# Kernel optimization log

Measured on AMD Instinct MI355X. Metric: run time of the kernel, lower is better.

The kernel has to match this reference:

```python
import jax, jax.numpy as jnp
import numpy as np

DIM = 256
NUM_HEADS = 8
WINDOW = 8


def setup_inputs() -> dict:
    key = jax.random.key(0)
    k1, k2, k3 = jax.random.split(key, 3)
    x = jax.random.normal(k1, (4, DIM, 256, 256), dtype=jnp.float32)
    w_qkv = jax.random.normal(k2, (3 * DIM, DIM), dtype=jnp.float32) * 0.02
    w_proj = jax.random.normal(k3, (DIM, DIM), dtype=jnp.float32) * 0.02
    return {"x": x, "w_qkv": w_qkv, "w_proj": w_proj}


def reference(x, w_qkv, w_proj):
    B, C, H, W = x.shape
    ws = WINDOW
    nh = NUM_HEADS
    hd = C // nh
    scale = float(hd) ** -0.5

    pad_h = (ws - H % ws) % ws
    pad_w = (ws - W % ws) % ws
    if pad_h or pad_w:
        x = jnp.pad(x, ((0, 0), (0, 0), (0, pad_h), (0, pad_w)))
    Hp, Wp = H + pad_h, W + pad_w
    nHw, nWw = Hp // ws, Wp // ws
    N = ws * ws

    # 1x1 conv QKV projection (no bias): [3C,C] x [B,C,Hp,Wp]
    qkv = jnp.einsum('oc,bchw->bohw', w_qkv, x)
    q, k, v = jnp.split(qkv, 3, axis=1)

    def partition(t):
        # [B,C,Hp,Wp] -> [B*nHw*nWw, nh, N, hd]
        t = t.reshape(B, nh, hd, nHw, ws, nWw, ws)
        t = t.transpose(0, 3, 5, 1, 4, 6, 2)  # B,nHw,nWw,nh,ws,ws,hd
        return t.reshape(B * nHw * nWw, nh, N, hd)

    qw = partition(q)
    kw = partition(k)
    vw = partition(v)

    attn = jnp.einsum('whnd,whmd->whnm', qw, kw) * scale
    attn = jax.nn.softmax(attn, axis=-1)
    out = jnp.einsum('whnm,whmd->whnd', attn, vw)  # [Bn, nh, N, hd]

    # unpartition: [Bn,nh,N,hd] -> [B,C,Hp,Wp]
    out = out.reshape(B, nHw, nWw, nh, ws, ws, hd)
    out = out.transpose(0, 3, 6, 1, 4, 2, 5)  # B,nh,hd,nHw,ws,nWw,ws
    out = out.reshape(B, C, Hp, Wp)

    out = jnp.einsum('oc,bchw->bohw', w_proj, out)
    if pad_h:
        out = out[:, :, :H, :]
    if pad_w:
        out = out[:, :, :, :W]
    return out
```

## Files before the change

kernel.cpp:

```cpp
#include <hip/hip_runtime.h>


#define DIMC 256
#define NH   8
#define HD   32
#define WS   8
#define NTOK 64
#define HRES 256
#define IMG  (HRES * HRES)

#define XPITCH 272

typedef _Float16 f16x8 __attribute__((ext_vector_type(8)));
typedef _Float16 f16x4 __attribute__((ext_vector_type(4)));
typedef float    f32x4 __attribute__((ext_vector_type(4)));

#define MFMA(a, b, c) __builtin_amdgcn_mfma_f32_16x16x32_f16((a), (b), (c), 0, 0, 0)

__global__ __launch_bounds__(256) void cvt_weights(const float* __restrict__ wqkv,
                                                   const float* __restrict__ wproj,
                                                   _Float16* __restrict__ wq,
                                                   _Float16* __restrict__ wp)
{
    int i = blockIdx.x * 256 + threadIdx.x;
    const int NQ = 768 * 256;
    const int NT = NQ + 256 * 256;
    if (i < NQ)      wq[i] = (_Float16)wqkv[i];
    else if (i < NT) wp[i - NQ] = (_Float16)wproj[i - NQ];
}

template <int PRE>
__device__ __forceinline__ f16x8 ldw(const void* w, int idx)
{
    if constexpr (PRE) {
        return *(const f16x8*)((const _Float16*)w + idx);
    } else {
        const float* p = (const float*)w + idx;
        f16x8 r;
        #pragma unroll
        for (int j = 0; j < 8; ++j) r[j] = (_Float16)p[j];
        return r;
    }
}

__device__ __forceinline__ int2 shfl2(int2 v, int s)
{
    v.x = __shfl(v.x, s);
    v.y = __shfl(v.y, s);
    return v;
}

__device__ __forceinline__ int2 pack4(f32x4 a)
{
    f16x4 h;
    h[0] = (_Float16)a[0]; h[1] = (_Float16)a[1];
    h[2] = (_Float16)a[2]; h[3] = (_Float16)a[3];
    return __builtin_bit_cast(int2, h);
}

__device__ __forceinline__ f16x8 cat8(int2 lo, int2 hi)
{
    int4 w = {lo.x, lo.y, hi.x, hi.y};
    return __builtin_bit_cast(f16x8, w);
}

__device__ __forceinline__ f16x8 bfrag(int2 pu0, int2 pu1, int ln, int lq)
{
    const int slo = ln + 32 * (lq & 1);
    int2 l0 = shfl2(pu0, slo), h0 = shfl2(pu0, slo + 16);
    int2 l1 = shfl2(pu1, slo), h1 = shfl2(pu1, slo + 16);
    int2 lo = (lq & 2) ? l1 : l0;
    int2 hi = (lq & 2) ? h1 : h0;
    return cat8(lo, hi);
}

template <int PRE>
__global__ __launch_bounds__(512, 4)
void win_attn_mfma(const float* __restrict__ x,
                   const void* __restrict__ wqkv,
                   const void* __restrict__ wproj,
                   float* __restrict__ out)
{
    __shared__ _Float16 x_t[NTOK][XPITCH];
    __shared__ _Float16 ao_t[NTOK][XPITCH];

    const int t  = threadIdx.x;
    const int ln = t & 15;
    const int lq = (t & 63) >> 4;
    const int gu = __builtin_amdgcn_readfirstlane(t >> 6);

    const int lin = blockIdx.x + (blockIdx.y << 5) + (blockIdx.z << 10);
    const int w   = ((lin & 7) << 9) | (lin >> 3);
    const int b   = w >> 10;
    const int y0  = ((w >> 5) & 31) * WS;
    const int x0  = (w & 31) * WS;

    const f32x4 zero = {0.f, 0.f, 0.f, 0.f};
    const float scale = 0.17677669529663687f;

    {
        const int py = t & 7;
        const int cg = (t & 63) >> 3;
        const float* xb = x + (long)b * DIMC * IMG + (long)(y0 + py) * HRES + x0;
        #pragma unroll
        for (int i = 0; i < 4; ++i) {
            const int cbase = i * 64 + gu * 8;
            const float* src = xb + (long)(cbase + cg) * IMG;
            float4 f0 = *(const float4*)src;
            float4 f1 = *(const float4*)(src + 4);
            float v[8] = {f0.x, f0.y, f0.z, f0.w, f1.x, f1.y, f1.z, f1.w};
            #pragma unroll
            for (int s = 1; s < 8; s <<= 1) {
                float nv[8];
                #pragma unroll
                for (int j = 0; j < 8; ++j) {
                    float ex = __shfl_xor(v[j ^ s], 8 * s);
                    nv[j] = ((j ^ cg) & s) ? ex : v[j];
                }
                #pragma unroll
                for (int j = 0; j < 8; ++j) v[j] = nv[j];
            }
            f16x8 hv;
            #pragma unroll
            for (int j = 0; j < 8; ++j) hv[j] = (_Float16)v[j];
            *(f16x8*)&x_t[8 * py + cg][cbase] = hv;
        }
    }
    __syncthreads();

    int2 Qp[2][4], Kp[2][4], Vp[4][2];
    #pragma unroll
    for (int mt = 0; mt < 2; ++mt) {
        f32x4 aq[4], ak[4], av[4];
        #pragma unroll
        for (int nt = 0; nt < 4; ++nt) { aq[nt] = zero; ak[nt] = zero; av[nt] = zero; }
        const int rq = (          gu * HD + 16 * mt + ln) * DIMC;
        const int rk = (DIMC    + gu * HD + 16 * mt + ln) * DIMC;
        const int rv = (2 * DIMC + gu * HD + 16 * mt + ln) * DIMC;
        #pragma unroll
        for (int ks = 0; ks < 8; ++ks) {
            const int co = 32 * ks + 8 * lq;
            f16x8 wqf = ldw<PRE>(wqkv, rq + co);
            f16x8 wkf = ldw<PRE>(wqkv, rk + co);
            f16x8 wvf = ldw<PRE>(wqkv, rv + co);
            #pragma unroll
            for (int nt = 0; nt < 4; ++nt) {
                f16x8 xf = *(const f16x8*)&x_t[16 * nt + ln][co];
                aq[nt] = MFMA(wqf, xf, aq[nt]);
                ak[nt] = MFMA(wkf, xf, ak[nt]);
                av[nt] = MFMA(xf, wvf, av[nt]);
            }
        }
        #pragma unroll
        for (int nt = 0; nt < 4; ++nt) {
            Qp[mt][nt] = pack4(aq[nt] * scale);
            Kp[mt][nt] = pack4(ak[nt]);
            Vp[nt][mt] = pack4(av[nt]);
        }
    }

    {
        f16x8 kf[4], qf[4];
        #pragma unroll
        for (int kt = 0; kt < 4; ++kt) kf[kt] = bfrag(Kp[0][kt], Kp[1][kt], ln, lq);
        #pragma unroll
        for (int qt = 0; qt < 4; ++qt) qf[qt] = bfrag(Qp[0][qt], Qp[1][qt], ln, lq);

        f32x4 s[4][4];
        #pragma unroll
        for (int kt = 0; kt < 4; ++kt)
            #pragma unroll
            for (int qt = 0; qt < 4; ++qt)
                s[kt][qt] = MFMA(kf[kt], qf[qt], zero);

        float inv[4];
        #pragma unroll
        for (int qt = 0; qt < 4; ++qt) {
            float m = -1e30f;
            #pragma unroll
            for (int kt = 0; kt < 4; ++kt)
                #pragma unroll
                for (int r = 0; r < 4; ++r) m = fmaxf(m, s[kt][qt][r]);
            m = fmaxf(m, __shfl_xor(m, 16));
            m = fmaxf(m, __shfl_xor(m, 32));
            float sum = 0.f;
            #pragma unroll
            for (int kt = 0; kt < 4; ++kt)
                #pragma unroll
                for (int r = 0; r < 4; ++r) {
                    float e = __expf(s[kt][qt][r] - m);
                    s[kt][qt][r] = e;
                    sum += e;
                }
            sum += __shfl_xor(sum, 16);
            sum += __shfl_xor(sum, 32);
            inv[qt] = 1.f / sum;
        }

        int2 Pp[4][4];
        #pragma unroll
        for (int kt = 0; kt < 4; ++kt)
            #pragma unroll
            for (int qt = 0; qt < 4; ++qt)
                Pp[kt][qt] = pack4(s[kt][qt] * inv[qt]);

        f32x4 pv[2][4];
        #pragma unroll
        for (int dt = 0; dt < 2; ++dt)
            #pragma unroll
            for (int qt = 0; qt < 4; ++qt) pv[dt][qt] = zero;
        #pragma unroll
        for (int ks = 0; ks < 2; ++ks) {
            f16x8 vf[2], pf[4];
            #pragma unroll
            for (int dt = 0; dt < 2; ++dt)
                vf[dt] = bfrag(Vp[2 * ks][dt], Vp[2 * ks + 1][dt], ln, lq);
            #pragma unroll
            for (int qt = 0; qt < 4; ++qt)
                pf[qt] = bfrag(Pp[2 * ks][qt], Pp[2 * ks + 1][qt], ln, lq);
            #pragma unroll
            for (int dt = 0; dt < 2; ++dt)
                #pragma unroll
                for (int qt = 0; qt < 4; ++qt)
                    pv[dt][qt] = MFMA(vf[dt], pf[qt], pv[dt][qt]);
        }

        #pragma unroll
        for (int dt = 0; dt < 2; ++dt)
            #pragma unroll
            for (int qt = 0; qt < 4; ++qt) {
                f16x4 hv;
                #pragma unroll
                for (int r = 0; r < 4; ++r) hv[r] = (_Float16)pv[dt][qt][r];
                *(f16x4*)&ao_t[16 * qt + ln][gu * HD + 16 * dt + 4 * lq] = hv;
            }
    }
    __syncthreads();

    f32x4 fa[2][4];
    #pragma unroll
    for (int o = 0; o < 2; ++o)
        #pragma unroll
        for (int nt = 0; nt < 4; ++nt) fa[o][nt] = zero;
    {
        const int r0 = (16 * (2 * gu + 0) + ln) * DIMC;
        const int r1 = (16 * (2 * gu + 1) + ln) * DIMC;
        #pragma unroll
        for (int ks = 0; ks < 8; ++ks) {
            const int co = 32 * ks + 8 * lq;
            f16x8 w0 = ldw<PRE>(wproj, r0 + co);
            f16x8 w1 = ldw<PRE>(wproj, r1 + co);
            #pragma unroll
            for (int nt = 0; nt < 4; ++nt) {
                f16x8 af = *(const f16x8*)&ao_t[16 * nt + ln][co];
                fa[0][nt] = MFMA(w0, af, fa[0][nt]);
                fa[1][nt] = MFMA(w1, af, fa[1][nt]);
            }
        }
    }

    {
        float* ob = out + (long)b * DIMC * IMG + (long)y0 * HRES + x0;
        #pragma unroll
        for (int o = 0; o < 2; ++o)
            #pragma unroll
            for (int nt = 0; nt < 4; ++nt) {
                const int och = 16 * (2 * gu + o) + 4 * lq;
                const int tok = 16 * nt + ln;
                float* op = ob + (long)och * IMG + (tok >> 3) * HRES + (tok & 7);
                #pragma unroll
                for (int r = 0; r < 4; ++r) op[(long)r * IMG] = fa[o][nt][r];
            }
    }
}

extern "C" void kernel_launch(void* const* d_in, const int* in_sizes, int n_in,
                              void* d_out, int out_size, void* d_ws, size_t ws_size,
                              hipStream_t stream)
{
    const float* x      = (const float*)d_in[0];
    const float* w_qkv  = (const float*)d_in[1];
    const float* w_proj = (const float*)d_in[2];
    float* out          = (float*)d_out;

    dim3 grid(HRES / WS, HRES / WS, 4);
    dim3 block(512);

    const size_t need = (size_t)(768 * 256 + 256 * 256) * sizeof(_Float16);
    if (d_ws && ws_size >= need) {
        _Float16* wq = (_Float16*)d_ws;
        _Float16* wp = wq + 768 * 256;
        hipLaunchKernelGGL(cvt_weights, dim3(1024), dim3(256), 0, stream,
                           w_qkv, w_proj, wq, wp);
        hipLaunchKernelGGL((win_attn_mfma<1>), grid, block, 0, stream,
                           x, (const void*)wq, (const void*)wp, out);
    } else {
        hipLaunchKernelGGL((win_attn_mfma<0>), grid, block, 0, stream,
                           x, (const void*)w_qkv, (const void*)w_proj, out);
    }
}
```

Before: 1.013 ms.

## Process two adjacent windows per block with shared swizzled LDS buffer

Each block now handles two horizontally adjacent 8x8 windows, which halves the grid. The QKV weight fragments are reloaded per window, but the output-projection weights are loaded once and applied to 128 tokens. The separate x and attention-output LDS arrays are merged into one XOR-swizzled buffer that the attention output overwrites in place, and the global x loads and output stores now span 16 contiguous floats per row. In exchange, more register pressure from the doubled projection accumulators and extra barriers between the per-window phases may reduce overlap.

```diff
diff --git a/kernel.cpp b/kernel.cpp
--- a/kernel.cpp
+++ b/kernel.cpp
@@ -4,12 +4,10 @@
 #define DIMC 256
 #define NH   8
 #define HD   32
-#define WS   8
-#define NTOK 64
+#define NTOK2 128
 #define HRES 256
 #define IMG  (HRES * HRES)
-
-#define XPITCH 272
+#define XP   264
 
 typedef _Float16 f16x8 __attribute__((ext_vector_type(8)));
 typedef _Float16 f16x4 __attribute__((ext_vector_type(4)));
@@ -74,6 +72,11 @@
     return cat8(lo, hi);
 }
 
+__device__ __forceinline__ int swz(int row, int col)
+{
+    return row * XP + (col ^ (((row >> 3) & 7) << 3));
+}
+
 template <int PRE>
 __global__ __launch_bounds__(512, 4)
 void win_attn_mfma(const float* __restrict__ x,
@@ -81,31 +84,31 @@
                    const void* __restrict__ wproj,
                    float* __restrict__ out)
 {
-    __shared__ _Float16 x_t[NTOK][XPITCH];
-    __shared__ _Float16 ao_t[NTOK][XPITCH];
+    __shared__ _Float16 xa[NTOK2 * XP];
 
     const int t  = threadIdx.x;
     const int ln = t & 15;
     const int lq = (t & 63) >> 4;
     const int gu = __builtin_amdgcn_readfirstlane(t >> 6);
 
-    const int lin = blockIdx.x + (blockIdx.y << 5) + (blockIdx.z << 10);
-    const int w   = ((lin & 7) << 9) | (lin >> 3);
-    const int b   = w >> 10;
-    const int y0  = ((w >> 5) & 31) * WS;
-    const int x0  = (w & 31) * WS;
+    const int lin = blockIdx.x + (blockIdx.y << 4) + (blockIdx.z << 9);
+    const int w   = ((lin & 7) << 8) | (lin >> 3);
+    const int b   = w >> 9;
+    const int y0  = ((w >> 4) & 31) * 8;
+    const int x0  = (w & 15) * 16;
 
     const f32x4 zero = {0.f, 0.f, 0.f, 0.f};
     const float scale = 0.17677669529663687f;
 
     {
         const int py = t & 7;
-        const int cg = (t & 63) >> 3;
+        const int cg = (t >> 3) & 7;
         const float* xb = x + (long)b * DIMC * IMG + (long)(y0 + py) * HRES + x0;
         #pragma unroll
-        for (int i = 0; i < 4; ++i) {
-            const int cbase = i * 64 + gu * 8;
-            const float* src = xb + (long)(cbase + cg) * IMG;
+        for (int i = 0; i < 8; ++i) {
+            const int win = i & 1;
+            const int cb  = (i >> 1) * 64 + gu * 8;
+            const float* src = xb + (long)(cb + cg) * IMG + win * 8;
             float4 f0 = *(const float4*)src;
             float4 f1 = *(const float4*)(src + 4);
             float v[8] = {f0.x, f0.y, f0.z, f0.w, f1.x, f1.y, f1.z, f1.w};
@@ -123,43 +126,45 @@
             f16x8 hv;
             #pragma unroll
             for (int j = 0; j < 8; ++j) hv[j] = (_Float16)v[j];
-            *(f16x8*)&x_t[8 * py + cg][cbase] = hv;
-        }
-    }
-    __syncthreads();
+            *(f16x8*)&xa[swz(win * 64 + 8 * py + cg, cb)] = hv;
+        }
+    }
 
     int2 Qp[2][4], Kp[2][4], Vp[4][2];
-    #pragma unroll
-    for (int mt = 0; mt < 2; ++mt) {
-        f32x4 aq[4], ak[4], av[4];
-        #pragma unroll
-        for (int nt = 0; nt < 4; ++nt) { aq[nt] = zero; ak[nt] = zero; av[nt] = zero; }
-        const int rq = (          gu * HD + 16 * mt + ln) * DIMC;
-        const int rk = (DIMC    + gu * HD + 16 * mt + ln) * DIMC;
-        const int rv = (2 * DIMC + gu * HD + 16 * mt + ln) * DIMC;
-        #pragma unroll
-        for (int ks = 0; ks < 8; ++ks) {
-            const int co = 32 * ks + 8 * lq;
-            f16x8 wqf = ldw<PRE>(wqkv, rq + co);
-            f16x8 wkf = ldw<PRE>(wqkv, rk + co);
-            f16x8 wvf = ldw<PRE>(wqkv, rv + co);
+
+    auto qkv_win = [&](int win) {
+        #pragma unroll
+        for (int mt = 0; mt < 2; ++mt) {
+            f32x4 aq[4], ak[4], av[4];
+            #pragma unroll
+            for (int nt = 0; nt < 4; ++nt) { aq[nt] = zero; ak[nt] = zero; av[nt] = zero; }
+            const int rq = (gu * HD + 16 * mt + ln) * DIMC;
+            const int rk = rq + DIMC * DIMC;
+            const int rv = rk + DIMC * DIMC;
+            #pragma unroll
+            for (int ks = 0; ks < 8; ++ks) {
+                const int co = 32 * ks + 8 * lq;
+                f16x8 wqf = ldw<PRE>(wqkv, rq + co);
+                f16x8 wkf = ldw<PRE>(wqkv, rk + co);
+                f16x8 wvf = ldw<PRE>(wqkv, rv + co);
+                #pragma unroll
+                for (int nt = 0; nt < 4; ++nt) {
+                    f16x8 xf = *(const f16x8*)&xa[swz(win * 64 + 16 * nt + ln, co)];
+                    aq[nt] = MFMA(wqf, xf, aq[nt]);
+                    ak[nt] = MFMA(wkf, xf, ak[nt]);
+                    av[nt] = MFMA(xf, wvf, av[nt]);
+                }
+            }
             #pragma unroll
             for (int nt = 0; nt < 4; ++nt) {
-                f16x8 xf = *(const f16x8*)&x_t[16 * nt + ln][co];
-                aq[nt] = MFMA(wqf, xf, aq[nt]);
-                ak[nt] = MFMA(wkf, xf, ak[nt]);
-                av[nt] = MFMA(xf, wvf, av[nt]);
-            }
-        }
-        #pragma unroll
-        for (int nt = 0; nt < 4; ++nt) {
-            Qp[mt][nt] = pack4(aq[nt] * scale);
-            Kp[mt][nt] = pack4(ak[nt]);
-            Vp[nt][mt] = pack4(av[nt]);
-        }
-    }
-
-    {
+                Qp[mt][nt] = pack4(aq[nt] * scale);
+                Kp[mt][nt] = pack4(ak[nt]);
+                Vp[nt][mt] = pack4(av[nt]);
+            }
+        }
+    };
+
+    auto attn_win = [&](int win) {
         f16x8 kf[4], qf[4];
         #pragma unroll
         for (int kt = 0; kt < 4; ++kt) kf[kt] = bfrag(Kp[0][kt], Kp[1][kt], ln, lq);
@@ -232,16 +237,25 @@
                 f16x4 hv;
                 #pragma unroll
                 for (int r = 0; r < 4; ++r) hv[r] = (_Float16)pv[dt][qt][r];
-                *(f16x4*)&ao_t[16 * qt + ln][gu * HD + 16 * dt + 4 * lq] = hv;
-            }
-    }
+                *(f16x4*)&xa[swz(win * 64 + 16 * qt + ln,
+                                 gu * HD + 16 * dt + 4 * lq)] = hv;
+            }
+    };
+
     __syncthreads();
-
-    f32x4 fa[2][4];
+    qkv_win(0);
+    __syncthreads();
+    attn_win(0);
+    qkv_win(1);
+    __syncthreads();
+    attn_win(1);
+    __syncthreads();
+
+    f32x4 fa[2][8];
     #pragma unroll
     for (int o = 0; o < 2; ++o)
         #pragma unroll
-        for (int nt = 0; nt < 4; ++nt) fa[o][nt] = zero;
+        for (int nt = 0; nt < 8; ++nt) fa[o][nt] = zero;
     {
         const int r0 = (16 * (2 * gu + 0) + ln) * DIMC;
         const int r1 = (16 * (2 * gu + 1) + ln) * DIMC;
@@ -251,8 +265,8 @@
             f16x8 w0 = ldw<PRE>(wproj, r0 + co);
             f16x8 w1 = ldw<PRE>(wproj, r1 + co);
             #pragma unroll
-            for (int nt = 0; nt < 4; ++nt) {
-                f16x8 af = *(const f16x8*)&ao_t[16 * nt + ln][co];
+            for (int nt = 0; nt < 8; ++nt) {
+                f16x8 af = *(const f16x8*)&xa[swz(16 * nt + ln, co)];
                 fa[0][nt] = MFMA(w0, af, fa[0][nt]);
                 fa[1][nt] = MFMA(w1, af, fa[1][nt]);
             }
@@ -264,10 +278,11 @@
         #pragma unroll
         for (int o = 0; o < 2; ++o)
             #pragma unroll
-            for (int nt = 0; nt < 4; ++nt) {
+            for (int nt = 0; nt < 8; ++nt) {
                 const int och = 16 * (2 * gu + o) + 4 * lq;
                 const int tok = 16 * nt + ln;
-                float* op = ob + (long)och * IMG + (tok >> 3) * HRES + (tok & 7);
+                const int win = tok >> 6, py = (tok >> 3) & 7, px = tok & 7;
+                float* op = ob + (long)och * IMG + py * HRES + win * 8 + px;
                 #pragma unroll
                 for (int r = 0; r < 4; ++r) op[(long)r * IMG] = fa[o][nt][r];
             }
@@ -283,7 +298,7 @@
     const float* w_proj = (const float*)d_in[2];
     float* out          = (float*)d_out;
 
-    dim3 grid(HRES / WS, HRES / WS, 4);
+    dim3 grid(HRES / 16, HRES / 8, 4);
     dim3 block(512);
 
     const size_t need = (size_t)(768 * 256 + 256 * 256) * sizeof(_Float16);
```

After: 1.325 ms. 1.31x slower.
